# Kernel optimization log

Hardware: AMD Instinct MI355X
Metric: run time of the kernel (lower is better)

Reference implementation:

```python
import jax, jax.numpy as jnp
import numpy as np

BS, C_IN, C_OUT, K, STYLE_DIM, BANK = 8, 64, 64, 3, 512, 4
D = H = W = 32
EPS = 1e-8
STRIDE = 1
PAD = 1


def setup_inputs() -> dict:
    key = jax.random.key(0)
    ks = jax.random.split(key, 7)
    lim_f = 1.0 / np.sqrt(STYLE_DIM)
    return {
        "x": jax.random.normal(ks[0], (BS, C_IN, D, H, W), dtype=jnp.float32),
        "w": jax.random.normal(ks[1], (BS, STYLE_DIM), dtype=jnp.float32),
        "filter_w": jax.random.uniform(ks[2], (BANK, STYLE_DIM), jnp.float32, -lim_f, lim_f),
        "filter_b": jax.random.uniform(ks[3], (BANK,), jnp.float32, -lim_f, lim_f),
        "mod_w": jax.random.uniform(ks[4], (C_IN, STYLE_DIM), jnp.float32, -lim_f, lim_f),
        "mod_b": jax.random.uniform(ks[5], (C_IN,), jnp.float32, -lim_f, lim_f),
        "bank": jax.random.normal(ks[6], (BANK, C_OUT, C_IN, K, K, K), dtype=jnp.float32),
    }


def reference(x, w, filter_w, filter_b, mod_w, mod_b, bank):
    bs, c_in, d, h, ww = x.shape
    # bank selection weights: softmax over bank axis
    fwt = jax.nn.softmax(w @ filter_w.T + filter_b, axis=-1)          # [bs, bank]
    # per-sample weights from bank (bank layout: n, out, in, k, k, k)
    weighted = jnp.einsum('bn,noijkl->boijkl', fwt, bank)             # [bs, out, in, k, k, k]
    # style modulation over input channels
    mod = (w @ mod_w.T + mod_b).reshape(bs, 1, c_in, 1, 1, 1)
    mw = weighted * mod
    # demodulation: normalize each (sample, out-channel) filter
    demod = jax.lax.rsqrt(jnp.sum(mw * mw, axis=(2, 3, 4, 5), keepdims=True) + EPS)
    mw = mw * demod
    # grouped conv with groups = bs
    mw = mw.reshape(bs * C_OUT, c_in, K, K, K)
    xr = x.reshape(1, bs * c_in, d, h, ww)
    out = jax.lax.conv_general_dilated(
        xr, mw,
        window_strides=(STRIDE,) * 3,
        padding=[(PAD, PAD)] * 3,
        dimension_numbers=('NCDHW', 'OIDHW', 'NCDHW'),
        feature_group_count=bs,
    )
    return out.reshape(bs, C_OUT, out.shape[-3], out.shape[-2], out.shape[-1])
```

## Files before the change

kernel.cpp:

```cpp
#include <hip/hip_runtime.h>
#include <math.h>

#define BS 8
#define CIN 64
#define COUT 64
#define SDIM 512
#define NBANK 4
#define DSZ 32
#define SPATIAL (DSZ*DSZ*DSZ)
#define NTAP 27
#define CH 8
#define NCH 8
#define NST 14
#define SLABTEX (1124*33)
#define WINTEX 3301
#define XBUFT 3304
#define ABUFT 1792
#define A3PERB (NCH*NST*128)
#define XP_TEXELS (64*SLABTEX)
constexpr float EPS = 1e-8f;

typedef short bf16x8 __attribute__((ext_vector_type(8)));
typedef float f32x16 __attribute__((ext_vector_type(16)));

__device__ __forceinline__ unsigned pack2(float a, float b) {
    unsigned ua = __float_as_uint(a);
    unsigned ub = __float_as_uint(b);
    ua = (ua + 0x7fffu + ((ua >> 16) & 1u)) >> 16;
    ub = (ub + 0x7fffu + ((ub >> 16) & 1u)) & 0xffff0000u;
    return ua | ub;
}
__device__ __forceinline__ unsigned short bf16r(float f) {
    unsigned u = __float_as_uint(f);
    u = (u + 0x7fffu + ((u >> 16) & 1u)) >> 16;
    return (unsigned short)u;
}
__device__ __forceinline__ void gload_lds16(const int4* g, int4* l) {
    __builtin_amdgcn_global_load_lds(
        (const __attribute__((address_space(1))) unsigned int*)(const void*)g,
        (__attribute__((address_space(3))) unsigned int*)(void*)l, 16, 0, 0);
}

__global__ __launch_bounds__(256) void prep_fused(
        const float* __restrict__ x,
        const float* __restrict__ w,
        const float* __restrict__ filter_w,
        const float* __restrict__ filter_b,
        const float* __restrict__ mod_w,
        const float* __restrict__ mod_b,
        const float* __restrict__ bank,
        int4* __restrict__ xP,
        unsigned short* __restrict__ wA3) {
    const int gid = blockIdx.x;
    const int t   = threadIdx.x;

    if (gid < 128) {
        const int b   = gid >> 4;
        const int oc  = (gid & 15) * 4 + (t >> 6);
        const int ic  = t & 63;
        const float* wb = w + b * SDIM;

        float fw[NBANK];
#pragma unroll
        for (int n = 0; n < NBANK; ++n) {
            float p = 0.0f;
            const float* fr = filter_w + n * SDIM;
#pragma unroll
            for (int k = 0; k < 8; ++k) p += wb[ic + 64 * k] * fr[ic + 64 * k];
#pragma unroll
            for (int off = 32; off >= 1; off >>= 1) p += __shfl_xor(p, off, 64);
            fw[n] = p + filter_b[n];
        }
        float mx = fmaxf(fmaxf(fw[0], fw[1]), fmaxf(fw[2], fw[3]));
        float se = 0.0f;
#pragma unroll
        for (int n = 0; n < NBANK; ++n) { fw[n] = expf(fw[n] - mx); se += fw[n]; }
        const float inv = 1.0f / se;
        const float f0 = fw[0] * inv, f1 = fw[1] * inv, f2 = fw[2] * inv, f3 = fw[3] * inv;

        float m = mod_b[ic];
        {
            const float4* wv4 = (const float4*)wb;
            const float4* mr4 = (const float4*)(mod_w + ic * SDIM);
            for (int j = 0; j < SDIM / 4; ++j) {
                float4 a = wv4[j], c = mr4[j];
                m += a.x * c.x + a.y * c.y + a.z * c.z + a.w * c.w;
            }
        }

        const float* b0 = bank + (size_t)((0 * COUT + oc) * CIN + ic) * NTAP;
        const float* b1 = bank + (size_t)((1 * COUT + oc) * CIN + ic) * NTAP;
        const float* b2 = bank + (size_t)((2 * COUT + oc) * CIN + ic) * NTAP;
        const float* b3 = bank + (size_t)((3 * COUT + oc) * CIN + ic) * NTAP;

        float v[NTAP];
        float ss = 0.0f;
#pragma unroll
        for (int k = 0; k < NTAP; ++k) {
            float tv = f0 * b0[k] + f1 * b1[k] + f2 * b2[k] + f3 * b3[k];
            tv *= m;
            v[k] = tv;
            ss += tv * tv;
        }
#pragma unroll
        for (int off = 32; off >= 1; off >>= 1) ss += __shfl_xor(ss, off, 64);
        const float d = rsqrtf(ss + EPS);

        const int c_  = ic >> 3, icl = ic & 7;
        const int at_ = oc >> 5, ln_ = oc & 31;
#pragma unroll
        for (int k = 0; k < 28; ++k) {
            const float val = (k < NTAP) ? v[k] * d : 0.0f;
            const size_t tex = ((size_t)(b * NCH + c_) * NST + (k >> 1)) * 128
                             + (size_t)at_ * 64 + (size_t)(k & 1) * 32 + ln_;
            wA3[tex * 8 + icl] = bf16r(val);
        }
    } else {
        const int j2   = gid - 128;
        const int zidx = j2 % 34;
        const int ch   = (j2 / 34) & 7;
        const int b    = j2 / 272;
        int4* slab = xP + (size_t)(b * NCH + ch) * SLABTEX;
        const int4 z4 = make_int4(0, 0, 0, 0);

        if (zidx >= 32) {
            const int base = (zidx == 32) ? 0 : 1090 * 33;
            for (int p = t; p < 34 * 33; p += 256) slab[base + p] = z4;
            return;
        }
        const float* xc = x + ((size_t)b * CIN + ch * CH) * SPATIAL + zidx * 1024;
        int4* dst = slab + (34 + 33 * zidx) * 33;
        for (int p = t; p < 33 * 33; p += 256) {
            const int r  = p / 33;
            const int cx = p - r * 33;
            int4 vv = z4;
            if (r < 32 && cx > 0) {
                const float* s = xc + r * 32 + (cx - 1);
                vv.x = (int)pack2(s[0 * SPATIAL], s[1 * SPATIAL]);
                vv.y = (int)pack2(s[2 * SPATIAL], s[3 * SPATIAL]);
                vv.z = (int)pack2(s[4 * SPATIAL], s[5 * SPATIAL]);
                vv.w = (int)pack2(s[6 * SPATIAL], s[7 * SPATIAL]);
            }
            dst[p] = vv;
        }
    }
}

__global__ __launch_bounds__(512, 2) void conv3d_mfma(
        const int4* __restrict__ xP,
        const int4* __restrict__ wA3,
        float* __restrict__ out) {
    const int bid = blockIdx.x;
    const int b = bid & 7, z = bid >> 3;
    const int t    = threadIdx.x;
    const int l    = t & 63;
    const int ln31 = t & 31;
    const int h2   = (t >> 5) & 1;
    const int wv   = t >> 6;

    __shared__ int4 smem[2 * XBUFT + 2 * ABUFT];

    int offB[NST];
#pragma unroll
    for (int s = 0; s < NST; ++s) {
        int tap = 2 * s + h2;
        if (tap > 26) tap = 0;
        const int dz = tap / 9, r = tap - dz * 9, dy = r / 3, dx = r - dy * 3;
        offB[s] = (dz * 1089 + dy * 33 + dx) * 16;
    }
    int baseB[4];
#pragma unroll
    for (int st = 0; st < 4; ++st)
        baseB[st] = ((wv * 4 + st) * 33 + ln31) * 16;

    auto stage = [&](int c, int buf) {
        const int4* xsrc = xP + (size_t)(b * NCH + c) * SLABTEX + (size_t)z * 1089;
        const int4* asrc = wA3 + (size_t)(b * NCH + c) * ABUFT;
        int4* lx = smem + buf * XBUFT;
        int4* la = smem + 2 * XBUFT + buf * ABUFT;
#pragma unroll
        for (int i = 0; i < 7; ++i) {
            const int p = i * 512 + t;
            if (p < WINTEX) gload_lds16(xsrc + p, lx + (p & ~63));
        }
#pragma unroll
        for (int i = 0; i < 4; ++i) {
            const int p = i * 512 + t;
            if (p < ABUFT) gload_lds16(asrc + p, la + (p & ~63));
        }
    };

    f32x16 acc[2][4];
#pragma unroll
    for (int i = 0; i < 2; ++i)
#pragma unroll
        for (int j = 0; j < 4; ++j)
#pragma unroll
            for (int r = 0; r < 16; ++r) acc[i][j][r] = 0.0f;

    stage(0, 0);
    __syncthreads();

    for (int c = 0; c < NCH; ++c) {
        if (c + 1 < NCH) stage(c + 1, (c + 1) & 1);
        const char* Xb = (const char*)(smem + (c & 1) * XBUFT);
        const char* Ab = (const char*)(smem + 2 * XBUFT + (c & 1) * ABUFT);
#pragma unroll
        for (int s = 0; s < NST; ++s) {
            bf16x8 a[2];
#pragma unroll
            for (int at = 0; at < 2; ++at)
                a[at] = *(const bf16x8*)(Ab + s * 2048 + at * 1024 + l * 16);
            bf16x8 bfr[4];
#pragma unroll
            for (int st = 0; st < 4; ++st)
                bfr[st] = *(const bf16x8*)(Xb + baseB[st] + offB[s]);
            __builtin_amdgcn_s_setprio(1);
#pragma unroll
            for (int at = 0; at < 2; ++at)
#pragma unroll
                for (int st = 0; st < 4; ++st)
                    acc[at][st] = __builtin_amdgcn_mfma_f32_32x32x16_bf16(
                        a[at], bfr[st], acc[at][st], 0, 0, 0);
            __builtin_amdgcn_s_setprio(0);
        }
        __syncthreads();
    }

    float* ob = out + (size_t)b * COUT * SPATIAL + (size_t)z * 1024;
#pragma unroll
    for (int at = 0; at < 2; ++at)
#pragma unroll
        for (int st = 0; st < 4; ++st) {
            const int sp = (wv * 4 + st) * 32 + ln31;
#pragma unroll
            for (int r = 0; r < 16; ++r) {
                const int oc = at * 32 + (r & 3) + 8 * (r >> 2) + 4 * h2;
                ob[(size_t)oc * SPATIAL + sp] = acc[at][st][r];
            }
        }
}

extern "C" void kernel_launch(void* const* d_in, const int* in_sizes, int n_in,
                              void* d_out, int out_size, void* d_ws, size_t ws_size,
                              hipStream_t stream) {
    const float* x        = (const float*)d_in[0];
    const float* w        = (const float*)d_in[1];
    const float* filter_w = (const float*)d_in[2];
    const float* filter_b = (const float*)d_in[3];
    const float* mod_w    = (const float*)d_in[4];
    const float* mod_b    = (const float*)d_in[5];
    const float* bank     = (const float*)d_in[6];
    float* out = (float*)d_out;

    int4* xP = (int4*)d_ws;
    unsigned short* wA3 = (unsigned short*)(xP + XP_TEXELS);

    prep_fused<<<128 + 34 * 8 * 8, 256, 0, stream>>>(
        x, w, filter_w, filter_b, mod_w, mod_b, bank, xP, wA3);
    conv3d_mfma<<<256, 512, 0, stream>>>(xP, (const int4*)wA3, out);
}
```

Measured before the change: 86.58 us.

## Reorder weight taps so B fragments are reused across dy in conv MFMA loop

```diff
diff --git a/kernel.cpp b/kernel.cpp
--- a/kernel.cpp
+++ b/kernel.cpp
@@ -16,7 +16,6 @@
 #define WINTEX 3301
 #define XBUFT 3304
 #define ABUFT 1792
-#define A3PERB (NCH*NST*128)
 #define XP_TEXELS (64*SLABTEX)
 constexpr float EPS = 1e-8f;
 
@@ -108,12 +107,21 @@
 
         const int c_  = ic >> 3, icl = ic & 7;
         const int at_ = oc >> 5, ln_ = oc & 31;
-#pragma unroll
-        for (int k = 0; k < 28; ++k) {
-            const float val = (k < NTAP) ? v[k] * d : 0.0f;
-            const size_t tex = ((size_t)(b * NCH + c_) * NST + (k >> 1)) * 128
-                             + (size_t)at_ * 64 + (size_t)(k & 1) * 32 + ln_;
-            wA3[tex * 8 + icl] = bf16r(val);
+        const size_t abase = (size_t)(b * NCH + c_) * NST * 128
+                           + (size_t)at_ * 64 + ln_;
+#pragma unroll
+        for (int k = 0; k < NTAP; ++k) {
+            const int dz = k / 9, r9 = k - dz * 9, dy = r9 / 3, dx = r9 - dy * 3;
+            const int j  = dz * 3 + dx;
+            int mm, hh;
+            if (j < 8) { mm = 3 * (j >> 1) + dy; hh = j & 1; }
+            else       { mm = (dy == 2) ? 13 : 12; hh = (dy == 1) ? 1 : 0; }
+            const size_t tex = abase + (size_t)mm * 128 + (size_t)hh * 32;
+            wA3[tex * 8 + icl] = bf16r(v[k] * d);
+        }
+        {
+            const size_t tex = abase + (size_t)13 * 128 + 32;
+            wA3[tex * 8 + icl] = 0;
         }
     } else {
         const int j2   = gid - 128;
@@ -160,18 +168,17 @@
 
     __shared__ int4 smem[2 * XBUFT + 2 * ABUFT];
 
-    int offB[NST];
-#pragma unroll
-    for (int s = 0; s < NST; ++s) {
-        int tap = 2 * s + h2;
-        if (tap > 26) tap = 0;
-        const int dz = tap / 9, r = tap - dz * 9, dy = r / 3, dx = r - dy * 3;
-        offB[s] = (dz * 1089 + dy * 33 + dx) * 16;
+    int rowQ[6];
+#pragma unroll
+    for (int q = 0; q < 6; ++q)
+        rowQ[q] = ((wv * 4 + q) * 33 + ln31) * 16;
+    int offc[4];
+#pragma unroll
+    for (int s = 0; s < 4; ++s) {
+        const int j = 2 * s + h2;
+        offc[s] = ((j / 3) * 1089 + (j % 3)) * 16;
     }
-    int baseB[4];
-#pragma unroll
-    for (int st = 0; st < 4; ++st)
-        baseB[st] = ((wv * 4 + st) * 33 + ln31) * 16;
+    const int off8 = (2 * 1089 + 2) * 16;
 
     auto stage = [&](int c, int buf) {
         const int4* xsrc = xP + (size_t)(b * NCH + c) * SLABTEX + (size_t)z * 1089;
@@ -205,24 +212,69 @@
         if (c + 1 < NCH) stage(c + 1, (c + 1) & 1);
         const char* Xb = (const char*)(smem + (c & 1) * XBUFT);
         const char* Ab = (const char*)(smem + 2 * XBUFT + (c & 1) * ABUFT);
-#pragma unroll
-        for (int s = 0; s < NST; ++s) {
-            bf16x8 a[2];
-#pragma unroll
-            for (int at = 0; at < 2; ++at)
-                a[at] = *(const bf16x8*)(Ab + s * 2048 + at * 1024 + l * 16);
-            bf16x8 bfr[4];
-#pragma unroll
-            for (int st = 0; st < 4; ++st)
-                bfr[st] = *(const bf16x8*)(Xb + baseB[st] + offB[s]);
-            __builtin_amdgcn_s_setprio(1);
-#pragma unroll
-            for (int at = 0; at < 2; ++at)
-#pragma unroll
-                for (int st = 0; st < 4; ++st)
-                    acc[at][st] = __builtin_amdgcn_mfma_f32_32x32x16_bf16(
-                        a[at], bfr[st], acc[at][st], 0, 0, 0);
-            __builtin_amdgcn_s_setprio(0);
+
+        auto mfma4 = [&](const bf16x8& a, const int4& Bf, int at) {
+        };
+        (void)mfma4;
+
+#pragma unroll
+        for (int s = 0; s < 4; ++s) {
+            int4 F[6];
+#pragma unroll
+            for (int q = 0; q < 6; ++q)
+                F[q] = *(const int4*)(Xb + rowQ[q] + offc[s]);
+            bf16x8 a0[2], a1[2], a2[2];
+#pragma unroll
+            for (int at = 0; at < 2; ++at) {
+                a0[at] = *(const bf16x8*)(Ab + (3 * s + 0) * 2048 + at * 1024 + l * 16);
+                a1[at] = *(const bf16x8*)(Ab + (3 * s + 1) * 2048 + at * 1024 + l * 16);
+                a2[at] = *(const bf16x8*)(Ab + (3 * s + 2) * 2048 + at * 1024 + l * 16);
+            }
+#pragma unroll
+            for (int at = 0; at < 2; ++at)
+#pragma unroll
+                for (int st = 0; st < 4; ++st)
+                    acc[at][st] = __builtin_amdgcn_mfma_f32_32x32x16_bf16(
+                        a0[at], *(const bf16x8*)&F[st], acc[at][st], 0, 0, 0);
+#pragma unroll
+            for (int at = 0; at < 2; ++at)
+#pragma unroll
+                for (int st = 0; st < 4; ++st)
+                    acc[at][st] = __builtin_amdgcn_mfma_f32_32x32x16_bf16(
+                        a1[at], *(const bf16x8*)&F[st + 1], acc[at][st], 0, 0, 0);
+#pragma unroll
+            for (int at = 0; at < 2; ++at)
+#pragma unroll
+                for (int st = 0; st < 4; ++st)
+                    acc[at][st] = __builtin_amdgcn_mfma_f32_32x32x16_bf16(
+                        a2[at], *(const bf16x8*)&F[st + 2], acc[at][st], 0, 0, 0);
+        }
+
+        {
+            int4 T1[4], T2[4];
+#pragma unroll
+            for (int st = 0; st < 4; ++st) {
+                T1[st] = *(const int4*)(Xb + rowQ[st] + h2 * (33 * 16) + off8);
+                T2[st] = *(const int4*)(Xb + rowQ[st + 2] + off8);
+            }
+            bf16x8 a12[2], a13[2];
+#pragma unroll
+            for (int at = 0; at < 2; ++at) {
+                a12[at] = *(const bf16x8*)(Ab + 12 * 2048 + at * 1024 + l * 16);
+                a13[at] = *(const bf16x8*)(Ab + 13 * 2048 + at * 1024 + l * 16);
+            }
+#pragma unroll
+            for (int at = 0; at < 2; ++at)
+#pragma unroll
+                for (int st = 0; st < 4; ++st)
+                    acc[at][st] = __builtin_amdgcn_mfma_f32_32x32x16_bf16(
+                        a12[at], *(const bf16x8*)&T1[st], acc[at][st], 0, 0, 0);
+#pragma unroll
+            for (int at = 0; at < 2; ++at)
+#pragma unroll
+                for (int st = 0; st < 4; ++st)
+                    acc[at][st] = __builtin_amdgcn_mfma_f32_32x32x16_bf16(
+                        a13[at], *(const bf16x8*)&T2[st], acc[at][st], 0, 0, 0);
         }
         __syncthreads();
     }
```

New measurement: 84.58 us. -2.3%, faster.
